# Kernel tuning notes

Measured on AMD Instinct MI355X. Metric: run time of the kernel, lower is better.

Reference implementation:

```python
import jax, jax.numpy as jnp
import numpy as np

D_MODEL = 1024
N_HEADS = 16
D_KEY = D_MODEL // N_HEADS


def setup_inputs() -> dict:
    key = jax.random.key(0)
    ks = jax.random.split(key, 11)
    s = 1.0 / np.sqrt(D_MODEL)
    inp = {
        'query': jax.random.normal(ks[0], (2, 2048, D_MODEL), dtype=jnp.float32),
        'key': jax.random.normal(ks[1], (2, 2048, D_MODEL), dtype=jnp.float32),
        'value': jax.random.normal(ks[2], (2, 2048, D_MODEL), dtype=jnp.float32),
        'Wq': jax.random.uniform(ks[3], (D_MODEL, D_MODEL), jnp.float32, -s, s),
        'bq': jax.random.uniform(ks[4], (D_MODEL,), jnp.float32, -s, s),
        'Wk': jax.random.uniform(ks[5], (D_MODEL, D_MODEL), jnp.float32, -s, s),
        'bk': jax.random.uniform(ks[6], (D_MODEL,), jnp.float32, -s, s),
        'Wv': jax.random.uniform(ks[7], (D_MODEL, D_MODEL), jnp.float32, -s, s),
        'bv': jax.random.uniform(ks[8], (D_MODEL,), jnp.float32, -s, s),
        'Wo': jax.random.uniform(ks[9], (D_MODEL, D_MODEL), jnp.float32, -s, s),
        'bo': jax.random.uniform(ks[10], (D_MODEL,), jnp.float32, -s, s),
    }
    return inp


def _split_heads(x):
    b, s, _ = x.shape
    return x.reshape(b, s, N_HEADS, D_KEY).transpose(0, 2, 1, 3)  # [b,h,s,dk]


def reference(query, key, value, Wq, bq, Wk, bk, Wv, bv, Wo, bo):
    q = _split_heads(query @ Wq.T + bq)
    k = _split_heads(key @ Wk.T + bk)
    v = _split_heads(value @ Wv.T + bv)
    scale = 1.0 / jnp.sqrt(jnp.float32(D_KEY))
    scores = jnp.einsum('bhqd,bhkd->bhqk', q, k) * scale  # [b,h,s,s]
    probs = jax.nn.softmax(scores, axis=-1)
    attn = jnp.einsum('bhqk,bhkd->bhqd', probs, v)
    b, h, s, dk = attn.shape
    combined = attn.transpose(0, 2, 1, 3).reshape(b, s, D_MODEL)
    return combined @ Wo.T + bo
```

## Files before the change

### kernel.cpp

```cpp
#include <hip/hip_runtime.h>
#include <hip/hip_bf16.h>

#define DEVI __device__ __forceinline__

typedef short bf16x8 __attribute__((ext_vector_type(8)));
typedef float f32x4  __attribute__((ext_vector_type(4)));

#define WS_XQ   0u
#define WS_XK   4194304u
#define WS_XV   8388608u
#define WS_WQ   12582912u
#define WS_WK   13631488u
#define WS_WV   14680064u
#define WS_WO   15728640u
#define WS_QB   16777216u
#define WS_KB   20971520u
#define WS_VT   25165824u
#define WS_CB   29360128u

#define QSCALE 0.18033688011112042f

DEVI short f2bf(float f) {
  union { float f; unsigned u; } c; c.f = f;
  return (short)((c.u + 0x8000u) >> 16);
}

DEVI unsigned pk2(float a, float b) {
  union { float f; unsigned u; } x, y; x.f = a; y.f = b;
  return ((x.u + 0x8000u) >> 16) | ((y.u + 0x8000u) & 0xffff0000u);
}

DEVI void async16(const short* g, const short* l) {
  __builtin_amdgcn_global_load_lds(
      (const __attribute__((address_space(1))) void*)g,
      (__attribute__((address_space(3))) void*)l, 16, 0, 0);
}

__global__ __launch_bounds__(256) void conv_kernel(
    const float* __restrict__ q, const float* __restrict__ k, const float* __restrict__ v,
    const float* __restrict__ Wq, const float* __restrict__ Wk,
    const float* __restrict__ Wv, const float* __restrict__ Wo,
    short* __restrict__ ws)
{
  size_t e = ((size_t)blockIdx.x * 256 + threadIdx.x) * 8;
  const float* src; short* dst; float sc = 1.0f;
  if (e < 12582912u) {
    size_t which = e >> 22;
    size_t off   = e & 4194303u;
    src = (which == 0 ? q : which == 1 ? k : v) + off;
    dst = ws + which * 4194304u + off;
  } else {
    size_t j = e - 12582912u;
    size_t which = j >> 20;
    size_t off   = j & 1048575u;
    src = (which == 0 ? Wq : which == 1 ? Wk : which == 2 ? Wv : Wo) + off;
    dst = ws + 12582912u + which * 1048576u + off;
    if (which == 0) sc = QSCALE;
  }
  float4 f0 = *(const float4*)src;
  float4 f1 = *(const float4*)(src + 4);
  int4 o;
  o.x = pk2(f0.x * sc, f0.y * sc);
  o.y = pk2(f0.z * sc, f0.w * sc);
  o.z = pk2(f1.x * sc, f1.y * sc);
  o.w = pk2(f1.z * sc, f1.w * sc);
  *(int4*)dst = o;
}

template <int BN>
DEVI void gemm_body(const short* __restrict__ A, const short* __restrict__ Bt,
                    const float* __restrict__ bias, void* __restrict__ C,
                    int outmode, float bscale)
{
  constexpr int Kd = 1024, Nd = 1024;
  constexpr int NT = BN / 32;
  __shared__ __attribute__((aligned(16))) short smem[2][4096 + BN * 32];

  const int tid  = threadIdx.x;
  const int lane = tid & 63;
  const int w    = tid >> 6;
  const int quad = lane >> 4, cl = lane & 15;
  const int m0 = blockIdx.y * 128, n0 = blockIdx.x * BN;
  const int wm = (w >> 1) * 64, wn = (w & 1) * (BN / 2);

  auto stage = [&](int k0, int buf) {
    short* Ab = &smem[buf][0];
    short* Bb = &smem[buf][4096];
#pragma unroll
    for (int i = 0; i < 2; ++i) {
      int f = (w * 2 + i) * 64 + lane;
      int r = f >> 2;
      int kb = (f & 3) ^ (r & 3) ^ ((r >> 2) & 1);
      async16(A + (size_t)(m0 + r) * Kd + k0 + kb * 8, Ab + f * 8);
    }
#pragma unroll
    for (int i = 0; i < BN / 64; ++i) {
      int f = (w * (BN / 64) + i) * 64 + lane;
      int r = f >> 2;
      int kb = (f & 3) ^ (r & 3) ^ ((r >> 2) & 1);
      async16(Bt + (size_t)(n0 + r) * Kd + k0 + kb * 8, Bb + f * 8);
    }
  };

  f32x4 acc[4][NT];
#pragma unroll
  for (int i = 0; i < 4; ++i)
#pragma unroll
    for (int j = 0; j < NT; ++j)
#pragma unroll
      for (int r = 0; r < 4; ++r) acc[i][j][r] = 0.0f;

  stage(0, 0);
  __builtin_amdgcn_s_waitcnt(0);
  __syncthreads();

  for (int j = 0; j < 32; ++j) {
    if (j < 31) stage((j + 1) * 32, (j + 1) & 1);
    const short* Ab = &smem[j & 1][0];
    const short* Bb = &smem[j & 1][4096];
    bf16x8 af[4], bfr[NT];
#pragma unroll
    for (int mt = 0; mt < 4; ++mt) {
      int r = wm + mt * 16 + cl;
      int off = r * 32 + ((quad ^ (r & 3) ^ ((r >> 2) & 1)) << 3);
      af[mt] = *(const bf16x8*)&Ab[off];
    }
#pragma unroll
    for (int nt = 0; nt < NT; ++nt) {
      int r = wn + nt * 16 + cl;
      int off = r * 32 + ((quad ^ (r & 3) ^ ((r >> 2) & 1)) << 3);
      bfr[nt] = *(const bf16x8*)&Bb[off];
    }
#pragma unroll
    for (int mt = 0; mt < 4; ++mt)
#pragma unroll
      for (int nt = 0; nt < NT; ++nt)
        acc[mt][nt] = __builtin_amdgcn_mfma_f32_16x16x32_bf16(af[mt], bfr[nt], acc[mt][nt], 0, 0, 0);
    __builtin_amdgcn_s_waitcnt(0);
    __syncthreads();
  }

  if (BN == 128 && outmode == 1) {
    short* flat = &smem[0][0];
#pragma unroll
    for (int mt = 0; mt < 4; ++mt)
#pragma unroll
      for (int nt = 0; nt < NT; ++nt) {
        int n_l = wn + nt * 16 + cl;
        float bv = bias[n0 + n_l] * bscale;
        int m_base = wm + mt * 16 + quad * 4;
        short4 pk;
        pk.x = f2bf(acc[mt][nt][0] + bv);
        pk.y = f2bf(acc[mt][nt][1] + bv);
        pk.z = f2bf(acc[mt][nt][2] + bv);
        pk.w = f2bf(acc[mt][nt][3] + bv);
        int u = m_base >> 2;
        int addr = n_l * 128 + ((u ^ (n_l & 31)) << 2);
        *(short4*)&flat[addr] = pk;
      }
    __syncthreads();
    short* Cs = (short*)C;
    int bb = m0 >> 11;
    int s0 = m0 & 2047;
#pragma unroll
    for (int p = 0; p < 4; ++p) {
      int n_l = w * 32 + p * 8 + (lane >> 3);
      int mb = (lane & 7) * 16;
      short4 t0, t1, t2, t3;
      {
        int u = (mb >> 2) + 0; t0 = *(short4*)&flat[n_l * 128 + ((u ^ (n_l & 31)) << 2)];
        u = (mb >> 2) + 1;     t1 = *(short4*)&flat[n_l * 128 + ((u ^ (n_l & 31)) << 2)];
        u = (mb >> 2) + 2;     t2 = *(short4*)&flat[n_l * 128 + ((u ^ (n_l & 31)) << 2)];
        u = (mb >> 2) + 3;     t3 = *(short4*)&flat[n_l * 128 + ((u ^ (n_l & 31)) << 2)];
      }
      size_t g = ((size_t)(bb * 1024 + n0 + n_l)) * 2048 + s0 + mb;
      *(short4*)&Cs[g]      = t0;
      *(short4*)&Cs[g + 4]  = t1;
      *(short4*)&Cs[g + 8]  = t2;
      *(short4*)&Cs[g + 12] = t3;
    }
    return;
  }

#pragma unroll
  for (int mt = 0; mt < 4; ++mt)
#pragma unroll
    for (int nt = 0; nt < NT; ++nt) {
      int n = n0 + wn + nt * 16 + cl;
      float bv = bias[n] * bscale;
#pragma unroll
      for (int r = 0; r < 4; ++r) {
        int m = m0 + wm + mt * 16 + quad * 4 + r;
        float val = acc[mt][nt][r] + bv;
        if (outmode == 2) ((float*)C)[(size_t)m * Nd + n] = val;
        else              ((short*)C)[(size_t)m * Nd + n] = f2bf(val);
      }
    }
}

__global__ __launch_bounds__(256, 3) void proj_gemm(
    short* ws, const float* __restrict__ bq, const float* __restrict__ bk,
    const float* __restrict__ bv)
{
  int z = blockIdx.z;
  const short* A; const short* W; const float* bias; void* C;
  int mode; float bscale = 1.0f;
  if (z == 0)      { A = ws + WS_XQ; W = ws + WS_WQ; bias = bq; C = ws + WS_QB; mode = 0; bscale = QSCALE; }
  else if (z == 1) { A = ws + WS_XK; W = ws + WS_WK; bias = bk; C = ws + WS_KB; mode = 0; }
  else             { A = ws + WS_XV; W = ws + WS_WV; bias = bv; C = ws + WS_VT; mode = 1; }
  gemm_body<128>(A, W, bias, C, mode, bscale);
}

__global__ __launch_bounds__(256, 3) void out_gemm(
    const short* __restrict__ ws, const float* __restrict__ bo, float* __restrict__ out)
{
  gemm_body<64>(ws + WS_CB, ws + WS_WO, bo, out, 2, 1.0f);
}

__global__ __launch_bounds__(512, 2) void flash_kernel(
    const short* __restrict__ Qb, const short* __restrict__ Kb,
    const short* __restrict__ Vt, short* __restrict__ comb)
{
  __shared__ __attribute__((aligned(16))) short QsPs[16384];
  __shared__ __attribute__((aligned(16))) short Ks[3][4096];
  __shared__ __attribute__((aligned(16))) short Vts[2][4096];

  const int tid = threadIdx.x, lane = tid & 63, w = tid >> 6;
  const int quad = lane >> 4, cl = lane & 15;
  const int b = blockIdx.z, h = blockIdx.y, q0 = blockIdx.x * 256;
  const int qrow_base = w * 32;

  const short* Qg = Qb + ((size_t)(b * 2048 + q0)) * 1024 + h * 64;
  const short* Kg = Kb + ((size_t)(b * 2048)) * 1024 + h * 64;
  const short* Vg = Vt + ((size_t)(b * 1024 + h * 64)) * 2048;

  auto stageK = [&](int j0, short* Kd) {
    int f = w * 64 + lane;
    int r = f >> 3;
    int kb = (f & 7) ^ (r & 7);
    async16(Kg + (size_t)(j0 + r) * 1024 + kb * 8, Kd + f * 8);
  };
  auto stageV = [&](int j0, short* Vd) {
    int f = w * 64 + lane;
    int r = f >> 3;
    int kb = (f & 7) ^ (r & 7);
    async16(Vg + (size_t)r * 2048 + j0 + kb * 8, Vd + f * 8);
  };

#pragma unroll
  for (int i = 0; i < 4; ++i) {
    int f = w * 256 + i * 64 + lane;
    int r = f >> 3, kb = (f & 7) ^ (r & 7);
    async16(Qg + (size_t)r * 1024 + kb * 8, QsPs + f * 8);
  }
  stageK(0, Ks[0]);
  stageK(64, Ks[1]);
  stageV(0, Vts[0]);
  __builtin_amdgcn_s_waitcnt(0);

  bf16x8 qa[2][2];
#pragma unroll
  for (int qt = 0; qt < 2; ++qt)
#pragma unroll
    for (int ks = 0; ks < 2; ++ks) {
      int r = qrow_base + qt * 16 + cl;
      int off = r * 64 + ((((ks << 2) | quad) ^ (r & 7)) << 3);
      qa[qt][ks] = *(const bf16x8*)&QsPs[off];
    }
  __syncthreads();

  auto qk = [&](const short* Kc, f32x4 (&dst)[4][2]) {
#pragma unroll
    for (int m = 0; m < 4; ++m)
#pragma unroll
      for (int qt = 0; qt < 2; ++qt)
#pragma unroll
        for (int r = 0; r < 4; ++r) dst[m][qt][r] = 0.0f;
#pragma unroll
    for (int ks = 0; ks < 2; ++ks) {
      bf16x8 ka[4];
#pragma unroll
      for (int m = 0; m < 4; ++m) {
        int r = m * 16 + cl;
        int off = r * 64 + ((((ks << 2) | quad) ^ (r & 7)) << 3);
        ka[m] = *(const bf16x8*)&Kc[off];
      }
#pragma unroll
      for (int m = 0; m < 4; ++m)
#pragma unroll
        for (int qt = 0; qt < 2; ++qt)
          dst[m][qt] = __builtin_amdgcn_mfma_f32_16x16x32_bf16(ka[m], qa[qt][ks], dst[m][qt], 0, 0, 0);
    }
  };

  f32x4 sA[4][2], sB[4][2];
  f32x4 accO[2][4];
  f32x4 accL[2];
#pragma unroll
  for (int qt = 0; qt < 2; ++qt) {
#pragma unroll
    for (int r = 0; r < 4; ++r) accL[qt][r] = 0.0f;
#pragma unroll
    for (int d = 0; d < 4; ++d)
#pragma unroll
      for (int r = 0; r < 4; ++r) accO[qt][d][r] = 0.0f;
  }

  const bf16x8 ones = { 0x3F80, 0x3F80, 0x3F80, 0x3F80, 0x3F80, 0x3F80, 0x3F80, 0x3F80 };

  qk(Ks[0], sA);

  int r0 = 0, r1 = 1, r2 = 2;
  auto body = [&](int j, f32x4 (&cur)[4][2], f32x4 (&nxt)[4][2]) {
    if (j + 2 < 32) stageK((j + 2) * 64, Ks[r2]);
    if (j + 1 < 32) { stageV((j + 1) * 64, Vts[(j + 1) & 1]); qk(Ks[r1], nxt); }
#pragma unroll
    for (int m = 0; m < 4; ++m)
#pragma unroll
      for (int qt = 0; qt < 2; ++qt) {
        int qrow = qrow_base + qt * 16 + cl;
        int u = m * 2 + (quad >> 1);
        int off = qrow * 64 + ((u ^ (qrow & 7)) << 3) + ((quad & 1) << 2);
        int2 pk;
        pk.x = pk2(__builtin_amdgcn_exp2f(cur[m][qt][0]),
                   __builtin_amdgcn_exp2f(cur[m][qt][1]));
        pk.y = pk2(__builtin_amdgcn_exp2f(cur[m][qt][2]),
                   __builtin_amdgcn_exp2f(cur[m][qt][3]));
        *(int2*)&QsPs[off] = pk;
      }
    const short* Vc = Vts[j & 1];
#pragma unroll
    for (int kt = 0; kt < 2; ++kt) {
      bf16x8 pa[2];
#pragma unroll
      for (int qt = 0; qt < 2; ++qt) {
        int qrow = qrow_base + qt * 16 + cl;
        int off = qrow * 64 + ((((kt << 2) | quad) ^ (qrow & 7)) << 3);
        pa[qt] = *(const bf16x8*)&QsPs[off];
        accL[qt] = __builtin_amdgcn_mfma_f32_16x16x32_bf16(pa[qt], ones, accL[qt], 0, 0, 0);
      }
#pragma unroll
      for (int d = 0; d < 4; ++d) {
        int rr = d * 16 + cl;
        int voff = rr * 64 + ((((kt << 2) | quad) ^ (rr & 7)) << 3);
        bf16x8 vb = *(const bf16x8*)&Vc[voff];
#pragma unroll
        for (int qt = 0; qt < 2; ++qt)
          accO[qt][d] = __builtin_amdgcn_mfma_f32_16x16x32_bf16(pa[qt], vb, accO[qt][d], 0, 0, 0);
      }
    }
    __builtin_amdgcn_s_waitcnt(0);
    __syncthreads();
    int t = r0; r0 = r1; r1 = r2; r2 = t;
  };

  for (int j = 0; j < 32; j += 2) {
    body(j, sA, sB);
    body(j + 1, sB, sA);
  }

#pragma unroll
  for (int qt = 0; qt < 2; ++qt) {
    float inv[4];
#pragma unroll
    for (int r = 0; r < 4; ++r) inv[r] = 1.0f / accL[qt][r];
#pragma unroll
    for (int d = 0; d < 4; ++d)
#pragma unroll
      for (int r = 0; r < 4; ++r) {
        int q = q0 + qrow_base + qt * 16 + quad * 4 + r;
        int dc = d * 16 + cl;
        comb[((size_t)(b * 2048 + q)) * 1024 + h * 64 + dc] = f2bf(accO[qt][d][r] * inv[r]);
      }
  }
}

extern "C" void kernel_launch(void* const* d_in, const int* in_sizes, int n_in,
                              void* d_out, int out_size, void* d_ws, size_t ws_size,
                              hipStream_t stream) {
  const float* q  = (const float*)d_in[0];
  const float* k  = (const float*)d_in[1];
  const float* v  = (const float*)d_in[2];
  const float* Wq = (const float*)d_in[3];
  const float* bq = (const float*)d_in[4];
  const float* Wk = (const float*)d_in[5];
  const float* bk = (const float*)d_in[6];
  const float* Wv = (const float*)d_in[7];
  const float* bv = (const float*)d_in[8];
  const float* Wo = (const float*)d_in[9];
  const float* bo = (const float*)d_in[10];
  short* ws = (short*)d_ws;
  float* out = (float*)d_out;

  conv_kernel<<<8192, 256, 0, stream>>>(q, k, v, Wq, Wk, Wv, Wo, ws);
  proj_gemm<<<dim3(8, 32, 3), 256, 0, stream>>>(ws, bq, bk, bv);
  flash_kernel<<<dim3(8, 16, 2), 512, 0, stream>>>(ws + WS_QB, ws + WS_KB, ws + WS_VT, ws + WS_CB);
  out_gemm<<<dim3(16, 32), 256, 0, stream>>>(ws, bo, out);
}
```

Before: 224.4 us.

## Load K/V directly from global into registers in flash kernel, drop LDS staging

The flash attention kernel no longer stages K and V tiles through shared memory with async copies and block barriers. Each wave now loads its K and V fragments straight from global memory into registers, with K double-buffered in registers. Blocks shrink to 256 threads and 128 query rows, doubling the grid. This removes the per-iteration __syncthreads and LDS traffic, but every wave now fetches the full K/V stream redundantly from global/L2 memory instead of sharing it through LDS.

```diff
diff --git a/kernel.cpp b/kernel.cpp
--- a/kernel.cpp
+++ b/kernel.cpp
@@ -217,83 +217,43 @@
   gemm_body<64>(ws + WS_CB, ws + WS_WO, bo, out, 2, 1.0f);
 }
 
-__global__ __launch_bounds__(512, 2) void flash_kernel(
+__global__ __launch_bounds__(256, 2) void flash_kernel(
     const short* __restrict__ Qb, const short* __restrict__ Kb,
     const short* __restrict__ Vt, short* __restrict__ comb)
 {
-  __shared__ __attribute__((aligned(16))) short QsPs[16384];
-  __shared__ __attribute__((aligned(16))) short Ks[3][4096];
-  __shared__ __attribute__((aligned(16))) short Vts[2][4096];
+  __shared__ __attribute__((aligned(16))) short Ps[8192];
 
   const int tid = threadIdx.x, lane = tid & 63, w = tid >> 6;
   const int quad = lane >> 4, cl = lane & 15;
-  const int b = blockIdx.z, h = blockIdx.y, q0 = blockIdx.x * 256;
+  const int b = blockIdx.z, h = blockIdx.y, q0 = blockIdx.x * 128;
   const int qrow_base = w * 32;
 
   const short* Qg = Qb + ((size_t)(b * 2048 + q0)) * 1024 + h * 64;
   const short* Kg = Kb + ((size_t)(b * 2048)) * 1024 + h * 64;
   const short* Vg = Vt + ((size_t)(b * 1024 + h * 64)) * 2048;
 
-  auto stageK = [&](int j0, short* Kd) {
-    int f = w * 64 + lane;
-    int r = f >> 3;
-    int kb = (f & 7) ^ (r & 7);
-    async16(Kg + (size_t)(j0 + r) * 1024 + kb * 8, Kd + f * 8);
+  bf16x8 qa[2][2];
+#pragma unroll
+  for (int qt = 0; qt < 2; ++qt)
+#pragma unroll
+    for (int ks = 0; ks < 2; ++ks)
+      qa[qt][ks] = *(const bf16x8*)(Qg + (size_t)(qrow_base + qt * 16 + cl) * 1024 + ks * 32 + quad * 8);
+
+  auto loadK = [&](int j0, bf16x8 (&ka)[4][2]) {
+#pragma unroll
+    for (int m = 0; m < 4; ++m)
+#pragma unroll
+      for (int ks = 0; ks < 2; ++ks)
+        ka[m][ks] = *(const bf16x8*)(Kg + (size_t)(j0 + m * 16 + cl) * 1024 + ks * 32 + quad * 8);
   };
-  auto stageV = [&](int j0, short* Vd) {
-    int f = w * 64 + lane;
-    int r = f >> 3;
-    int kb = (f & 7) ^ (r & 7);
-    async16(Vg + (size_t)r * 2048 + j0 + kb * 8, Vd + f * 8);
+  auto loadV = [&](int j0, bf16x8 (&vb)[2][4]) {
+#pragma unroll
+    for (int kt = 0; kt < 2; ++kt)
+#pragma unroll
+      for (int nt = 0; nt < 4; ++nt)
+        vb[kt][nt] = *(const bf16x8*)(Vg + (size_t)(nt * 16 + cl) * 2048 + j0 + kt * 32 + quad * 8);
   };
 
-#pragma unroll
-  for (int i = 0; i < 4; ++i) {
-    int f = w * 256 + i * 64 + lane;
-    int r = f >> 3, kb = (f & 7) ^ (r & 7);
-    async16(Qg + (size_t)r * 1024 + kb * 8, QsPs + f * 8);
-  }
-  stageK(0, Ks[0]);
-  stageK(64, Ks[1]);
-  stageV(0, Vts[0]);
-  __builtin_amdgcn_s_waitcnt(0);
-
-  bf16x8 qa[2][2];
-#pragma unroll
-  for (int qt = 0; qt < 2; ++qt)
-#pragma unroll
-    for (int ks = 0; ks < 2; ++ks) {
-      int r = qrow_base + qt * 16 + cl;
-      int off = r * 64 + ((((ks << 2) | quad) ^ (r & 7)) << 3);
-      qa[qt][ks] = *(const bf16x8*)&QsPs[off];
-    }
-  __syncthreads();
-
-  auto qk = [&](const short* Kc, f32x4 (&dst)[4][2]) {
-#pragma unroll
-    for (int m = 0; m < 4; ++m)
-#pragma unroll
-      for (int qt = 0; qt < 2; ++qt)
-#pragma unroll
-        for (int r = 0; r < 4; ++r) dst[m][qt][r] = 0.0f;
-#pragma unroll
-    for (int ks = 0; ks < 2; ++ks) {
-      bf16x8 ka[4];
-#pragma unroll
-      for (int m = 0; m < 4; ++m) {
-        int r = m * 16 + cl;
-        int off = r * 64 + ((((ks << 2) | quad) ^ (r & 7)) << 3);
-        ka[m] = *(const bf16x8*)&Kc[off];
-      }
-#pragma unroll
-      for (int m = 0; m < 4; ++m)
-#pragma unroll
-        for (int qt = 0; qt < 2; ++qt)
-          dst[m][qt] = __builtin_amdgcn_mfma_f32_16x16x32_bf16(ka[m], qa[qt][ks], dst[m][qt], 0, 0, 0);
-    }
-  };
-
-  f32x4 sA[4][2], sB[4][2];
   f32x4 accO[2][4];
   f32x4 accL[2];
 #pragma unroll
@@ -308,12 +268,29 @@
 
   const bf16x8 ones = { 0x3F80, 0x3F80, 0x3F80, 0x3F80, 0x3F80, 0x3F80, 0x3F80, 0x3F80 };
 
-  qk(Ks[0], sA);
-
-  int r0 = 0, r1 = 1, r2 = 2;
-  auto body = [&](int j, f32x4 (&cur)[4][2], f32x4 (&nxt)[4][2]) {
-    if (j + 2 < 32) stageK((j + 2) * 64, Ks[r2]);
-    if (j + 1 < 32) { stageV((j + 1) * 64, Vts[(j + 1) & 1]); qk(Ks[r1], nxt); }
+  bf16x8 kA[4][2], kB[4][2];
+  loadK(0, kA);
+
+  auto body = [&](int j, bf16x8 (&curK)[4][2], bf16x8 (&nxtK)[4][2]) {
+    if (j + 1 < 32) loadK((j + 1) * 64, nxtK);
+    bf16x8 vb[2][4];
+    loadV(j * 64, vb);
+
+    f32x4 s[4][2];
+#pragma unroll
+    for (int m = 0; m < 4; ++m)
+#pragma unroll
+      for (int qt = 0; qt < 2; ++qt)
+#pragma unroll
+        for (int r = 0; r < 4; ++r) s[m][qt][r] = 0.0f;
+#pragma unroll
+    for (int ks = 0; ks < 2; ++ks)
+#pragma unroll
+      for (int m = 0; m < 4; ++m)
+#pragma unroll
+        for (int qt = 0; qt < 2; ++qt)
+          s[m][qt] = __builtin_amdgcn_mfma_f32_16x16x32_bf16(curK[m][ks], qa[qt][ks], s[m][qt], 0, 0, 0);
+
 #pragma unroll
     for (int m = 0; m < 4; ++m)
 #pragma unroll
@@ -322,13 +299,13 @@
         int u = m * 2 + (quad >> 1);
         int off = qrow * 64 + ((u ^ (qrow & 7)) << 3) + ((quad & 1) << 2);
         int2 pk;
-        pk.x = pk2(__builtin_amdgcn_exp2f(cur[m][qt][0]),
-                   __builtin_amdgcn_exp2f(cur[m][qt][1]));
-        pk.y = pk2(__builtin_amdgcn_exp2f(cur[m][qt][2]),
-                   __builtin_amdgcn_exp2f(cur[m][qt][3]));
-        *(int2*)&QsPs[off] = pk;
-      }
-    const short* Vc = Vts[j & 1];
+        pk.x = pk2(__builtin_amdgcn_exp2f(s[m][qt][0]),
+                   __builtin_amdgcn_exp2f(s[m][qt][1]));
+        pk.y = pk2(__builtin_amdgcn_exp2f(s[m][qt][2]),
+                   __builtin_amdgcn_exp2f(s[m][qt][3]));
+        *(int2*)&Ps[off] = pk;
+      }
+
 #pragma unroll
     for (int kt = 0; kt < 2; ++kt) {
       bf16x8 pa[2];
@@ -336,27 +313,20 @@
       for (int qt = 0; qt < 2; ++qt) {
         int qrow = qrow_base + qt * 16 + cl;
         int off = qrow * 64 + ((((kt << 2) | quad) ^ (qrow & 7)) << 3);
-        pa[qt] = *(const bf16x8*)&QsPs[off];
+        pa[qt] = *(const bf16x8*)&Ps[off];
         accL[qt] = __builtin_amdgcn_mfma_f32_16x16x32_bf16(pa[qt], ones, accL[qt], 0, 0, 0);
       }
 #pragma unroll
-      for (int d = 0; d < 4; ++d) {
-        int rr = d * 16 + cl;
-        int voff = rr * 64 + ((((kt << 2) | quad) ^ (rr & 7)) << 3);
-        bf16x8 vb = *(const bf16x8*)&Vc[voff];
+      for (int d = 0; d < 4; ++d)
 #pragma unroll
         for (int qt = 0; qt < 2; ++qt)
-          accO[qt][d] = __builtin_amdgcn_mfma_f32_16x16x32_bf16(pa[qt], vb, accO[qt][d], 0, 0, 0);
-      }
-    }
-    __builtin_amdgcn_s_waitcnt(0);
-    __syncthreads();
-    int t = r0; r0 = r1; r1 = r2; r2 = t;
+          accO[qt][d] = __builtin_amdgcn_mfma_f32_16x16x32_bf16(pa[qt], vb[kt][d], accO[qt][d], 0, 0, 0);
+    }
   };
 
   for (int j = 0; j < 32; j += 2) {
-    body(j, sA, sB);
-    body(j + 1, sB, sA);
+    body(j, kA, kB);
+    body(j + 1, kB, kA);
   }
 
 #pragma unroll
@@ -394,6 +364,6 @@
 
   conv_kernel<<<8192, 256, 0, stream>>>(q, k, v, Wq, Wk, Wv, Wo, ws);
   proj_gemm<<<dim3(8, 32, 3), 256, 0, stream>>>(ws, bq, bk, bv);
-  flash_kernel<<<dim3(8, 16, 2), 512, 0, stream>>>(ws + WS_QB, ws + WS_KB, ws + WS_VT, ws + WS_CB);
+  flash_kernel<<<dim3(16, 16, 2), 256, 0, stream>>>(ws + WS_QB, ws + WS_KB, ws + WS_VT, ws + WS_CB);
   out_gemm<<<dim3(16, 32), 256, 0, stream>>>(ws, bo, out);
 }
```

Result: slower. 287.0 us (+27.9%).
